# Kernel optimization log

Measured on AMD Instinct MI355X. Metric: run time of the kernel, lower is better.

## Reference

```python
import jax, jax.numpy as jnp
import numpy as np

B, S, D = 2, 2048, 1024
E, K = 8, 2
H = 1792  # round_up(int(1024*5/3)=1706, 256)


def setup_inputs() -> dict:
    key = jax.random.key(0)
    k1, k2, k3, k4, k5 = jax.random.split(key, 5)
    scale = 0.02
    x = jax.random.normal(k1, (B, S, D), dtype=jnp.float32)
    gate_w = jax.random.normal(k2, (E, D), dtype=jnp.float32) * scale   # nn.Linear(D,E).weight
    w_gate = jax.random.normal(k3, (E, D, H), dtype=jnp.float32) * scale
    w_up = jax.random.normal(k4, (E, D, H), dtype=jnp.float32) * scale
    w_down = jax.random.normal(k5, (E, H, D), dtype=jnp.float32) * scale
    return {"x": x, "gate_w": gate_w, "w_gate": w_gate, "w_up": w_up, "w_down": w_down}


def reference(x, gate_w, w_gate, w_up, w_down):
    b, s, d = x.shape
    x_flat = x.reshape(-1, d)                      # [T, D]
    # Gate computed in bf16 (torch autocast) then cast back to f32.
    logits = (x_flat.astype(jnp.bfloat16) @ gate_w.T.astype(jnp.bfloat16)).astype(jnp.float32)  # [T, E]
    topk_w, topk_idx = jax.lax.top_k(logits, K)    # [T, K]
    topk_w = jax.nn.softmax(topk_w, axis=-1)
    probs = jax.nn.softmax(logits, axis=-1)        # [T, E]
    mean_probs = probs.mean(0)                     # [E]
    load_balance_loss = E * jnp.sum(mean_probs ** 2)
    # Per-token combine weight for each expert (equivalent to sort/split/index_add combine).
    combine = jnp.sum(jax.nn.one_hot(topk_idx, E, dtype=x_flat.dtype) * topk_w[..., None], axis=1)  # [T, E]
    out = jnp.zeros_like(x_flat)
    for e in range(E):  # fixed small expert loop; math identical to grouped dispatch
        g = x_flat @ w_gate[e]                     # [T, H]
        u = x_flat @ w_up[e]                       # [T, H]
        y = (jax.nn.silu(g) * u) @ w_down[e]       # [T, D]
        out = out + y * combine[:, e:e + 1]
    return out.reshape(b, s, d), load_balance_loss, mean_probs
```

## Files before the change

kernel.cpp:

```cpp
#include <hip/hip_runtime.h>
#include <stdint.h>

#define TT 4096
#define DD 1024
#define EE 8
#define HH 1792
#define MP 10240
#define MT256 40
#define MT128 80

typedef __attribute__((ext_vector_type(8))) short short8;
typedef __attribute__((ext_vector_type(4))) short short4v;
typedef __attribute__((ext_vector_type(4))) float f32x4;

static __device__ __forceinline__ unsigned short f2bf(float f) {
  union { float f; uint32_t u; } v; v.f = f;
  return (unsigned short)((v.u + 0x7fffu + ((v.u >> 16) & 1u)) >> 16);
}
static __device__ __forceinline__ float bf2f(unsigned short h) {
  union { uint32_t u; float f; } v; v.u = ((uint32_t)h) << 16;
  return v.f;
}

static __device__ __forceinline__ void gll16(const void* g, const void* l) {
  __builtin_amdgcn_global_load_lds(
      (const __attribute__((address_space(1))) unsigned int*)g,
      (__attribute__((address_space(3))) unsigned int*)l, 16, 0, 0);
}

__global__ __launch_bounds__(256) void transpose_convert(
    const float* __restrict__ in, unsigned short* __restrict__ outp, int R, int C,
    int ilv, int sel) {
  __shared__ float t[64][68];
  const float* src = in + (size_t)blockIdx.z * R * C + (size_t)(blockIdx.x * 64) * C +
                     blockIdx.y * 64;
  unsigned short* dst = outp + (size_t)blockIdx.z * R * C * (ilv ? 2 : 1);
  const int tid = threadIdx.x;
  const int lr = tid >> 2, lc = (tid & 3) * 16;
#pragma unroll
  for (int q = 0; q < 4; ++q) {
    const f32x4 v = *(const f32x4*)(src + (size_t)lr * C + lc + 4 * q);
    t[lr][lc + 4 * q + 0] = v[0]; t[lr][lc + 4 * q + 1] = v[1];
    t[lr][lc + 4 * q + 2] = v[2]; t[lr][lc + 4 * q + 3] = v[3];
  }
  __syncthreads();
  unsigned short b[16];
#pragma unroll
  for (int q = 0; q < 16; ++q) b[q] = f2bf(t[lc + q][lr]);
  const int cg = blockIdx.y * 64 + lr;
  const int prow = ilv ? ((cg >> 4) * 32 + sel * 16 + (cg & 15)) : cg;
  unsigned short* d = dst + (size_t)prow * R + blockIdx.x * 64 + lc;
  *(short8*)(d) = *(const short8*)&b[0];
  *(short8*)(d + 8) = *(const short8*)&b[8];
}

__global__ __launch_bounds__(256) void gate_kernel(
    const float* __restrict__ x, const float* __restrict__ gw,
    float* __restrict__ combine, float* __restrict__ probs, int2* __restrict__ topk) {
  const int lane = threadIdx.x & 63;
  const int wave = threadIdx.x >> 6;
  const int t = blockIdx.x * 4 + wave;
  const float* xr = x + (size_t)t * DD;
  float acc[EE];
#pragma unroll
  for (int e = 0; e < EE; ++e) acc[e] = 0.f;
  for (int i = 0; i < DD / 64; ++i) {
    const int d = i * 64 + lane;
    const float xv = bf2f(f2bf(xr[d]));
#pragma unroll
    for (int e = 0; e < EE; ++e)
      acc[e] += xv * bf2f(f2bf(gw[e * DD + d]));
  }
#pragma unroll
  for (int e = 0; e < EE; ++e) {
#pragma unroll
    for (int off = 32; off > 0; off >>= 1)
      acc[e] += __shfl_xor(acc[e], off, 64);
  }
  if (lane == 0) {
    float lg[EE];
#pragma unroll
    for (int e = 0; e < EE; ++e) lg[e] = bf2f(f2bf(acc[e]));
    float m1 = -1e30f, m2 = -1e30f; int i1 = 0, i2 = 0;
#pragma unroll
    for (int e = 0; e < EE; ++e) {
      const float v = lg[e];
      if (v > m1) { m2 = m1; i2 = i1; m1 = v; i1 = e; }
      else if (v > m2) { m2 = v; i2 = e; }
    }
    const float e2 = expf(m2 - m1);
    const float w1 = 1.f / (1.f + e2);
    const float w2 = e2 * w1;
    float cb[EE];
#pragma unroll
    for (int e = 0; e < EE; ++e) cb[e] = 0.f;
    cb[i1] = w1; cb[i2] += w2;
    float p[EE]; float s = 0.f;
#pragma unroll
    for (int e = 0; e < EE; ++e) { p[e] = expf(lg[e] - m1); s += p[e]; }
    const float inv = 1.f / s;
#pragma unroll
    for (int e = 0; e < EE; ++e) {
      combine[(size_t)t * EE + e] = cb[e];
      probs[(size_t)t * EE + e] = p[e] * inv;
    }
    topk[t] = make_int2(i1, i2);
  }
}

__global__ __launch_bounds__(256) void reduce_kernel(
    const float* __restrict__ probs, float* __restrict__ tail) {
  const int tid = threadIdx.x;
  const int lane = tid & 63, wave = tid >> 6;
  float acc[EE];
#pragma unroll
  for (int e = 0; e < EE; ++e) acc[e] = 0.f;
  for (int t = tid; t < TT; t += 256) {
#pragma unroll
    for (int e = 0; e < EE; ++e) acc[e] += probs[(size_t)t * EE + e];
  }
#pragma unroll
  for (int e = 0; e < EE; ++e) {
#pragma unroll
    for (int off = 32; off > 0; off >>= 1)
      acc[e] += __shfl_xor(acc[e], off, 64);
  }
  __shared__ float sm[4][EE];
  if (lane == 0) {
#pragma unroll
    for (int e = 0; e < EE; ++e) sm[wave][e] = acc[e];
  }
  __syncthreads();
  if (tid == 0) {
    float loss = 0.f;
#pragma unroll
    for (int e = 0; e < EE; ++e) {
      const float m = (sm[0][e] + sm[1][e] + sm[2][e] + sm[3][e]) * (1.f / TT);
      tail[1 + e] = m;
      loss += m * m;
    }
    tail[0] = (float)EE * loss;
  }
}

__global__ __launch_bounds__(512) void route_kernel(
    const int2* __restrict__ topk, const float* __restrict__ combine,
    int* __restrict__ tok_list, float* __restrict__ wt_list,
    int* __restrict__ tab256, int* __restrict__ tab128) {
  const int lane = threadIdx.x & 63;
  const int e = threadIdx.x >> 6;
  __shared__ int cnts[EE], offs[EE];
  int cnt = 0;
  for (int i = 0; i < TT / 64; ++i) {
    const int2 k2 = topk[i * 64 + lane];
    cnt += __popcll(__ballot(k2.x == e || k2.y == e));
  }
  if (lane == 0) cnts[e] = cnt;
  __syncthreads();
  if (threadIdx.x == 0) {
    int off = 0, n256 = 0, n128 = 0;
    for (int f = 0; f < EE; ++f) {
      offs[f] = off;
      const int pc = (cnts[f] + 255) & ~255;
      for (int j = 0; j < (pc >> 8); ++j) {
        tab256[2 * n256] = f; tab256[2 * n256 + 1] = off + 256 * j; ++n256;
      }
      for (int j = 0; j < (pc >> 7); ++j) {
        tab128[2 * n128] = f; tab128[2 * n128 + 1] = off + 128 * j; ++n128;
      }
      off += pc;
    }
    for (; n256 < MT256; ++n256) { tab256[2 * n256] = -1; tab256[2 * n256 + 1] = 0; }
    for (; n128 < MT128; ++n128) { tab128[2 * n128] = -1; tab128[2 * n128 + 1] = 0; }
  }
  __syncthreads();
  int pos = offs[e];
  for (int i = 0; i < TT / 64; ++i) {
    const int t = i * 64 + lane;
    const int2 k2 = topk[t];
    const bool sel = (k2.x == e || k2.y == e);
    const unsigned long long m = __ballot(sel);
    if (sel) {
      const int p = pos + __popcll(m & ((1ull << lane) - 1ull));
      tok_list[p] = t;
      wt_list[p] = combine[(size_t)t * EE + e];
    }
    pos += __popcll(m);
  }
  const int pc = (cnt + 255) & ~255;
  for (int s = cnt + lane; s < pc; s += 64) {
    tok_list[offs[e] + s] = 0;
    wt_list[offs[e] + s] = 0.f;
  }
}

__global__ __launch_bounds__(256) void gather_x(
    const float* __restrict__ x, const int* __restrict__ tok_list,
    const int* __restrict__ tab256, unsigned short* __restrict__ xg) {
  const int e = tab256[2 * blockIdx.x];
  if (e < 0) return;
  const int row0 = tab256[2 * blockIdx.x + 1] + blockIdx.y * 16;
  const int tid = threadIdx.x;
#pragma unroll
  for (int i = 0; i < 16; ++i) {
    const int row = row0 + i;
    const int tok = tok_list[row];
    const f32x4 v = *(const f32x4*)(x + (size_t)tok * DD + tid * 4);
    unsigned short b[4] = {f2bf(v[0]), f2bf(v[1]), f2bf(v[2]), f2bf(v[3])};
    *(short4v*)(xg + (size_t)row * DD + tid * 4) = *(const short4v*)b;
  }
}

template <int MODE>
__global__ __launch_bounds__(512, 2) void gemm_main(
    const unsigned short* __restrict__ Ab, const unsigned short* __restrict__ Bb,
    const int* __restrict__ tab, const int* __restrict__ tok_list,
    const float* __restrict__ wt_list, unsigned short* __restrict__ act,
    float* __restrict__ out) {
  constexpr int K      = (MODE == 0) ? DD : HH;
  constexpr int BM     = (MODE == 0) ? 256 : 128;
  constexpr int NBR    = (MODE == 0) ? 2 * HH : DD;
  constexpr int NK     = K / 32;
  constexpr int ABYTES = BM * 64;
  constexpr int SLOTB  = (BM + 256) * 64;
  constexpr int GLL    = SLOTB / 8192;
  constexpr int VCNT   = GLL;
  constexpr int NIT    = ((MODE == 0) ? 128 : 64) / 16;
  constexpr int NNT    = NBR / 256;
  extern __shared__ char lds[];

  const int nwg = gridDim.x;
  const int wgid = (blockIdx.x & 7) * (nwg >> 3) + (blockIdx.x >> 3);
  const int mt = wgid / NNT, nt = wgid % NNT;
  const int e = tab[2 * mt];
  if (e < 0) return;
  const int row0 = tab[2 * mt + 1];
  const int n0 = nt * 256;

  const int tid = threadIdx.x, lane = tid & 63, wave = tid >> 6;
  const int wm = (wave >> 2) * ((MODE == 0) ? 128 : 64);
  const int wn = (wave & 3) * 64;
  const int fr = lane & 15, hi = lane >> 4;

  const unsigned short* At = Ab + (size_t)row0 * K;
  const unsigned short* Bt = Bb + ((size_t)e * NBR + n0) * K;

  asm volatile("s_waitcnt vmcnt(0)" ::: "memory");

  auto stage_q = [&](int u, int slot, int q) {
    const int rel = q * 8192 + wave * 1024 + lane * 16;
    const bool isA = rel < ABYTES;
    const int rb = isA ? rel : rel - ABYTES;
    const int row = rb >> 6;
    const int l = (((rb >> 4) & 3)) ^ ((row >> 1) & 3);
    gll16((isA ? At : Bt) + (size_t)row * K + u * 32 + l * 8,
          lds + slot * SLOTB + q * 8192 + wave * 1024);
  };
  auto rdA = [&](int slot, int m) -> short8 {
    const int c = hi ^ ((m >> 1) & 3);
    return *(const short8*)(lds + slot * SLOTB + m * 64 + (c << 4));
  };
  auto rdB = [&](int slot, int n) -> short8 {
    const int c = hi ^ ((n >> 1) & 3);
    return *(const short8*)(lds + slot * SLOTB + ABYTES + n * 64 + (c << 4));
  };

  f32x4 acc[NIT][4];
#pragma unroll
  for (int i = 0; i < NIT; ++i)
#pragma unroll
    for (int j = 0; j < 4; ++j) acc[i][j] = (f32x4){0.f, 0.f, 0.f, 0.f};

#pragma unroll
  for (int q = 0; q < GLL; ++q) stage_q(0, 0, q);
#pragma unroll
  for (int q = 0; q < GLL; ++q) stage_q(1, 1, q);
  if constexpr (VCNT == 4) asm volatile("s_waitcnt vmcnt(4)" ::: "memory");
  else                     asm volatile("s_waitcnt vmcnt(3)" ::: "memory");
  __builtin_amdgcn_s_barrier();

  int slot = 0;
#pragma unroll 1
  for (int t = 0; t < NK; ++t) {
    const int nslot = (slot >= 1) ? slot - 1 : slot + 2;
    const int u = (t + 2 >= NK) ? t + 2 - NK : t + 2;
    short8 b[4];
    if constexpr (MODE == 0) {
      short8 a[4];
#pragma unroll
      for (int i = 0; i < 4; ++i) a[i] = rdA(slot, wm + i * 16 + fr);
#pragma unroll
      for (int j = 0; j < 4; ++j) b[j] = rdB(slot, wn + j * 16 + fr);
      stage_q(u, nslot, 0); stage_q(u, nslot, 1);
      __builtin_amdgcn_s_barrier();
      asm volatile("s_waitcnt lgkmcnt(0)" ::: "memory");
      __builtin_amdgcn_sched_barrier(0);
      __builtin_amdgcn_s_setprio(1);
#pragma unroll
      for (int i = 0; i < 4; ++i)
#pragma unroll
        for (int j = 0; j < 4; ++j)
          acc[i][j] = __builtin_amdgcn_mfma_f32_16x16x32_bf16(a[i], b[j], acc[i][j], 0, 0, 0);
      __builtin_amdgcn_s_setprio(0);
      __builtin_amdgcn_s_barrier();
#pragma unroll
      for (int i = 0; i < 4; ++i) a[i] = rdA(slot, wm + 64 + i * 16 + fr);
      stage_q(u, nslot, 2); stage_q(u, nslot, 3);
      asm volatile("s_waitcnt vmcnt(4)" ::: "memory");
      __builtin_amdgcn_s_barrier();
      asm volatile("s_waitcnt lgkmcnt(0)" ::: "memory");
      __builtin_amdgcn_sched_barrier(0);
      __builtin_amdgcn_s_setprio(1);
#pragma unroll
      for (int i = 0; i < 4; ++i)
#pragma unroll
        for (int j = 0; j < 4; ++j)
          acc[4 + i][j] = __builtin_amdgcn_mfma_f32_16x16x32_bf16(a[i], b[j], acc[4 + i][j], 0, 0, 0);
      __builtin_amdgcn_s_setprio(0);
      __builtin_amdgcn_s_barrier();
    } else {
      short8 a[4];
#pragma unroll
      for (int i = 0; i < 4; ++i) a[i] = rdA(slot, wm + i * 16 + fr);
#pragma unroll
      for (int j = 0; j < 2; ++j) b[j] = rdB(slot, wn + j * 16 + fr);
      stage_q(u, nslot, 0); stage_q(u, nslot, 1);
      __builtin_amdgcn_s_barrier();
      asm volatile("s_waitcnt lgkmcnt(0)" ::: "memory");
      __builtin_amdgcn_sched_barrier(0);
      __builtin_amdgcn_s_setprio(1);
#pragma unroll
      for (int i = 0; i < 4; ++i)
#pragma unroll
        for (int j = 0; j < 2; ++j)
          acc[i][j] = __builtin_amdgcn_mfma_f32_16x16x32_bf16(a[i], b[j], acc[i][j], 0, 0, 0);
      __builtin_amdgcn_s_setprio(0);
      __builtin_amdgcn_s_barrier();
#pragma unroll
      for (int j = 0; j < 2; ++j) b[2 + j] = rdB(slot, wn + 32 + j * 16 + fr);
      stage_q(u, nslot, 2);
      asm volatile("s_waitcnt vmcnt(3)" ::: "memory");
      __builtin_amdgcn_s_barrier();
      asm volatile("s_waitcnt lgkmcnt(0)" ::: "memory");
      __builtin_amdgcn_sched_barrier(0);
      __builtin_amdgcn_s_setprio(1);
#pragma unroll
      for (int i = 0; i < 4; ++i)
#pragma unroll
        for (int j = 0; j < 2; ++j)
          acc[i][2 + j] = __builtin_amdgcn_mfma_f32_16x16x32_bf16(a[i], b[2 + j], acc[i][2 + j], 0, 0, 0);
      __builtin_amdgcn_s_setprio(0);
      __builtin_amdgcn_s_barrier();
    }
    slot = (slot >= 2) ? 0 : slot + 1;
  }
  asm volatile("s_waitcnt vmcnt(0)" ::: "memory");

  const int r4 = hi * 4;
  if constexpr (MODE == 0) {
#pragma unroll
    for (int i = 0; i < NIT; ++i)
#pragma unroll
      for (int r = 0; r < 4; ++r) {
        const int row = row0 + wm + i * 16 + r4 + r;
#pragma unroll
        for (int jj = 0; jj < 2; ++jj) {
          const float g = acc[i][2 * jj][r], u = acc[i][2 * jj + 1][r];
          const int nb = n0 + wn + jj * 32;
          const int h = ((nb >> 5) << 4) + fr;
          act[(size_t)row * HH + h] = f2bf((g / (1.f + expf(-g))) * u);
        }
      }
  } else {
#pragma unroll
    for (int i = 0; i < NIT; ++i)
#pragma unroll
      for (int r = 0; r < 4; ++r) {
        const int rl = row0 + wm + i * 16 + r4 + r;
        const int tok = tok_list[rl];
        const float wt = wt_list[rl];
        if (wt != 0.f) {
#pragma unroll
          for (int j = 0; j < 4; ++j)
            unsafeAtomicAdd(&out[(size_t)tok * DD + n0 + wn + j * 16 + fr],
                            acc[i][j][r] * wt);
        }
      }
  }
}

extern "C" void kernel_launch(void* const* d_in, const int* in_sizes, int n_in,
                              void* d_out, int out_size, void* d_ws, size_t ws_size,
                              hipStream_t stream) {
  const float* x      = (const float*)d_in[0];
  const float* gw     = (const float*)d_in[1];
  const float* w_gate = (const float*)d_in[2];
  const float* w_up   = (const float*)d_in[3];
  const float* w_down = (const float*)d_in[4];
  float* out = (float*)d_out;
  float* tail = out + (size_t)TT * DD;

  char* w = (char*)d_ws;
  size_t o = 0;
  auto carve = [&](size_t bytes) { char* p = w + o; o += (bytes + 255) & ~255ull; return p; };
  unsigned short* wguT = (unsigned short*)carve((size_t)EE * 2 * HH * DD * 2);
  unsigned short* wdT  = (unsigned short*)carve((size_t)EE * DD * HH * 2);
  unsigned short* xg   = (unsigned short*)carve((size_t)MP * DD * 2);
  unsigned short* act  = (unsigned short*)carve((size_t)MP * HH * 2);
  float* combine = (float*)carve((size_t)TT * EE * 4);
  float* probs   = (float*)carve((size_t)TT * EE * 4);
  int2* topk     = (int2*)carve((size_t)TT * 8);
  int* tok_list  = (int*)carve((size_t)MP * 4);
  float* wt_list = (float*)carve((size_t)MP * 4);
  int* tab256    = (int*)carve((size_t)MT256 * 8);
  int* tab128    = (int*)carve((size_t)MT128 * 8);

  hipMemsetAsync(out, 0, (size_t)TT * DD * sizeof(float), stream);

  transpose_convert<<<dim3(DD / 64, HH / 64, EE), 256, 0, stream>>>(w_gate, wguT, DD, HH, 1, 0);
  transpose_convert<<<dim3(DD / 64, HH / 64, EE), 256, 0, stream>>>(w_up,   wguT, DD, HH, 1, 1);
  transpose_convert<<<dim3(HH / 64, DD / 64, EE), 256, 0, stream>>>(w_down, wdT,  HH, DD, 0, 0);

  gate_kernel<<<TT / 4, 256, 0, stream>>>(x, gw, combine, probs, topk);
  reduce_kernel<<<1, 256, 0, stream>>>(probs, tail);
  route_kernel<<<1, 512, 0, stream>>>(topk, combine, tok_list, wt_list, tab256, tab128);
  gather_x<<<dim3(MT256, 16), 256, 0, stream>>>(x, tok_list, tab256, xg);

  hipFuncSetAttribute(reinterpret_cast<const void*>(&gemm_main<0>),
                      hipFuncAttributeMaxDynamicSharedMemorySize, 98304);
  hipFuncSetAttribute(reinterpret_cast<const void*>(&gemm_main<1>),
                      hipFuncAttributeMaxDynamicSharedMemorySize, 73728);

  gemm_main<0><<<MT256 * 14, 512, 98304, stream>>>(xg, wguT, tab256, nullptr, nullptr, act, nullptr);
  gemm_main<1><<<MT128 * 4, 512, 73728, stream>>>(act, wdT, tab128, tok_list, wt_list, nullptr, out);
}
```

Before: 298.2 us.

## Restructure grouped GEMMs with K=64 double-buffered ping-pong pipeline and 256-row down tiles

```diff
diff --git a/kernel.cpp b/kernel.cpp
--- a/kernel.cpp
+++ b/kernel.cpp
@@ -7,7 +7,6 @@
 #define HH 1792
 #define MP 10240
 #define MT256 40
-#define MT128 80
 
 typedef __attribute__((ext_vector_type(8))) short short8;
 typedef __attribute__((ext_vector_type(4))) short short4v;
@@ -145,8 +144,7 @@
 
 __global__ __launch_bounds__(512) void route_kernel(
     const int2* __restrict__ topk, const float* __restrict__ combine,
-    int* __restrict__ tok_list, float* __restrict__ wt_list,
-    int* __restrict__ tab256, int* __restrict__ tab128) {
+    int* __restrict__ tok_list, float* __restrict__ wt_list, int* __restrict__ tab256) {
   const int lane = threadIdx.x & 63;
   const int e = threadIdx.x >> 6;
   __shared__ int cnts[EE], offs[EE];
@@ -158,20 +156,16 @@
   if (lane == 0) cnts[e] = cnt;
   __syncthreads();
   if (threadIdx.x == 0) {
-    int off = 0, n256 = 0, n128 = 0;
+    int off = 0, n256 = 0;
     for (int f = 0; f < EE; ++f) {
       offs[f] = off;
       const int pc = (cnts[f] + 255) & ~255;
       for (int j = 0; j < (pc >> 8); ++j) {
         tab256[2 * n256] = f; tab256[2 * n256 + 1] = off + 256 * j; ++n256;
       }
-      for (int j = 0; j < (pc >> 7); ++j) {
-        tab128[2 * n128] = f; tab128[2 * n128 + 1] = off + 128 * j; ++n128;
-      }
       off += pc;
     }
     for (; n256 < MT256; ++n256) { tab256[2 * n256] = -1; tab256[2 * n256 + 1] = 0; }
-    for (; n128 < MT128; ++n128) { tab128[2 * n128] = -1; tab128[2 * n128 + 1] = 0; }
   }
   __syncthreads();
   int pos = offs[e];
@@ -211,22 +205,34 @@
   }
 }
 
+#define PH_SYNC(VC)                                         \
+  __builtin_amdgcn_sched_barrier(0);                        \
+  asm volatile("s_waitcnt vmcnt(" #VC ")" ::: "memory");    \
+  __builtin_amdgcn_s_barrier();                             \
+  asm volatile("s_waitcnt lgkmcnt(0)" ::: "memory");        \
+  __builtin_amdgcn_sched_barrier(0);
+#define PH_SYNCN                                            \
+  __builtin_amdgcn_sched_barrier(0);                        \
+  __builtin_amdgcn_s_barrier();                             \
+  asm volatile("s_waitcnt lgkmcnt(0)" ::: "memory");        \
+  __builtin_amdgcn_sched_barrier(0);
+#define PH_END                                              \
+  __builtin_amdgcn_sched_barrier(0);                        \
+  __builtin_amdgcn_s_barrier();
+
 template <int MODE>
-__global__ __launch_bounds__(512, 2) void gemm_main(
+__global__ __launch_bounds__(512, 1) void gemm_main(
     const unsigned short* __restrict__ Ab, const unsigned short* __restrict__ Bb,
     const int* __restrict__ tab, const int* __restrict__ tok_list,
     const float* __restrict__ wt_list, unsigned short* __restrict__ act,
     float* __restrict__ out) {
-  constexpr int K      = (MODE == 0) ? DD : HH;
-  constexpr int BM     = (MODE == 0) ? 256 : 128;
-  constexpr int NBR    = (MODE == 0) ? 2 * HH : DD;
-  constexpr int NK     = K / 32;
-  constexpr int ABYTES = BM * 64;
-  constexpr int SLOTB  = (BM + 256) * 64;
-  constexpr int GLL    = SLOTB / 8192;
-  constexpr int VCNT   = GLL;
-  constexpr int NIT    = ((MODE == 0) ? 128 : 64) / 16;
-  constexpr int NNT    = NBR / 256;
+  constexpr int K    = (MODE == 0) ? DD : HH;
+  constexpr int NK   = K / 64;
+  constexpr int BN   = (MODE == 0) ? 256 : 128;
+  constexpr int NBR  = (MODE == 0) ? 2 * HH : DD;
+  constexpr int NNT  = NBR / BN;
+  constexpr int ABYT = 256 * 128;
+  constexpr int BUFB = ABYT + BN * 128;
   extern __shared__ char lds[];
 
   const int nwg = gridDim.x;
@@ -235,11 +241,11 @@
   const int e = tab[2 * mt];
   if (e < 0) return;
   const int row0 = tab[2 * mt + 1];
-  const int n0 = nt * 256;
+  const int n0 = nt * BN;
 
   const int tid = threadIdx.x, lane = tid & 63, wave = tid >> 6;
-  const int wm = (wave >> 2) * ((MODE == 0) ? 128 : 64);
-  const int wn = (wave & 3) * 64;
+  const int wm = (MODE == 0) ? (wave >> 2) * 128 : (wave >> 1) * 64;
+  const int wn = (MODE == 0) ? (wave & 3) * 64 : (wave & 1) * 64;
   const int fr = lane & 15, hi = lane >> 4;
 
   const unsigned short* At = Ab + (size_t)row0 * K;
@@ -247,112 +253,213 @@
 
   asm volatile("s_waitcnt vmcnt(0)" ::: "memory");
 
-  auto stage_q = [&](int u, int slot, int q) {
-    const int rel = q * 8192 + wave * 1024 + lane * 16;
-    const bool isA = rel < ABYTES;
-    const int rb = isA ? rel : rel - ABYTES;
-    const int row = rb >> 6;
-    const int l = (((rb >> 4) & 3)) ^ ((row >> 1) & 3);
-    gll16((isA ? At : Bt) + (size_t)row * K + u * 32 + l * 8,
-          lds + slot * SLOTB + q * 8192 + wave * 1024);
+  auto stage_half = [&](int u, int p, int h) {
+    const bool isA = (h < 2);
+    const unsigned short* src = isA ? At : Bt;
+    const int rbase = (h & 1) * 128;
+    const int lbase = p * BUFB + (isA ? 0 : ABYT) + rbase * 128;
+#pragma unroll
+    for (int q = 0; q < 2; ++q) {
+      const int rel = q * 8192 + wave * 1024 + lane * 16;
+      const int row = rel >> 7, ch = (rel >> 4) & 7;
+      gll16(src + (size_t)(rbase + row) * K + u * 64 + ((ch ^ (row & 7)) << 3),
+            lds + lbase + q * 8192 + wave * 1024);
+    }
   };
-  auto rdA = [&](int slot, int m) -> short8 {
-    const int c = hi ^ ((m >> 1) & 3);
-    return *(const short8*)(lds + slot * SLOTB + m * 64 + (c << 4));
+  auto rdA = [&](int p, int row, int kc) -> short8 {
+    const int lb = row * 128 + kc * 64 + hi * 16;
+    return *(const short8*)(lds + p * BUFB + (lb ^ ((row & 7) << 4)));
   };
-  auto rdB = [&](int slot, int n) -> short8 {
-    const int c = hi ^ ((n >> 1) & 3);
-    return *(const short8*)(lds + slot * SLOTB + ABYTES + n * 64 + (c << 4));
+  auto rdB = [&](int p, int row, int kc) -> short8 {
+    const int lb = row * 128 + kc * 64 + hi * 16;
+    return *(const short8*)(lds + p * BUFB + ABYT + (lb ^ ((row & 7) << 4)));
   };
 
+  constexpr int NIT = (MODE == 0) ? 8 : 4;
   f32x4 acc[NIT][4];
 #pragma unroll
   for (int i = 0; i < NIT; ++i)
 #pragma unroll
     for (int j = 0; j < 4; ++j) acc[i][j] = (f32x4){0.f, 0.f, 0.f, 0.f};
 
-#pragma unroll
-  for (int q = 0; q < GLL; ++q) stage_q(0, 0, q);
-#pragma unroll
-  for (int q = 0; q < GLL; ++q) stage_q(1, 1, q);
-  if constexpr (VCNT == 4) asm volatile("s_waitcnt vmcnt(4)" ::: "memory");
-  else                     asm volatile("s_waitcnt vmcnt(3)" ::: "memory");
+  if constexpr (MODE == 0) { stage_half(0, 0, 2); stage_half(0, 0, 3); }
+  else                     { stage_half(0, 0, 2); }
+  stage_half(0, 0, 0); stage_half(0, 0, 1);
+  asm volatile("s_waitcnt vmcnt(0)" ::: "memory");
   __builtin_amdgcn_s_barrier();
 
-  int slot = 0;
+  if constexpr (MODE == 0) {
+    short8 rB[2][4][2], rA03[4][2], rA47[2][4][2];
 #pragma unroll 1
-  for (int t = 0; t < NK; ++t) {
-    const int nslot = (slot >= 1) ? slot - 1 : slot + 2;
-    const int u = (t + 2 >= NK) ? t + 2 - NK : t + 2;
-    short8 b[4];
-    if constexpr (MODE == 0) {
-      short8 a[4];
-#pragma unroll
-      for (int i = 0; i < 4; ++i) a[i] = rdA(slot, wm + i * 16 + fr);
-#pragma unroll
-      for (int j = 0; j < 4; ++j) b[j] = rdB(slot, wn + j * 16 + fr);
-      stage_q(u, nslot, 0); stage_q(u, nslot, 1);
-      __builtin_amdgcn_s_barrier();
-      asm volatile("s_waitcnt lgkmcnt(0)" ::: "memory");
-      __builtin_amdgcn_sched_barrier(0);
-      __builtin_amdgcn_s_setprio(1);
-#pragma unroll
-      for (int i = 0; i < 4; ++i)
+    for (int tt = 0; tt < NK; tt += 2) {
+#pragma unroll
+      for (int par = 0; par < 2; ++par) {
+        const int t = tt + par;
+        const int p = par, pn = par ^ 1;
+        const int u = (t + 1 < NK) ? t + 1 : 0;
 #pragma unroll
         for (int j = 0; j < 4; ++j)
-          acc[i][j] = __builtin_amdgcn_mfma_f32_16x16x32_bf16(a[i], b[j], acc[i][j], 0, 0, 0);
-      __builtin_amdgcn_s_setprio(0);
-      __builtin_amdgcn_s_barrier();
-#pragma unroll
-      for (int i = 0; i < 4; ++i) a[i] = rdA(slot, wm + 64 + i * 16 + fr);
-      stage_q(u, nslot, 2); stage_q(u, nslot, 3);
-      asm volatile("s_waitcnt vmcnt(4)" ::: "memory");
-      __builtin_amdgcn_s_barrier();
-      asm volatile("s_waitcnt lgkmcnt(0)" ::: "memory");
-      __builtin_amdgcn_sched_barrier(0);
-      __builtin_amdgcn_s_setprio(1);
-#pragma unroll
-      for (int i = 0; i < 4; ++i)
+#pragma unroll
+          for (int kc = 0; kc < 2; ++kc) rB[p][j][kc] = rdB(p, wn + j * 16 + fr, kc);
+        stage_half(u, pn, 2);
+        PH_SYNC(2)
+        if (t > 0) {
+          __builtin_amdgcn_s_setprio(1);
+#pragma unroll
+          for (int i = 0; i < 4; ++i)
+#pragma unroll
+            for (int j = 0; j < 2; ++j)
+#pragma unroll
+              for (int kc = 0; kc < 2; ++kc)
+                acc[4 + i][j] = __builtin_amdgcn_mfma_f32_16x16x32_bf16(
+                    rA47[pn][i][kc], rB[pn][j][kc], acc[4 + i][j], 0, 0, 0);
+          __builtin_amdgcn_s_setprio(0);
+        }
+        PH_END
+#pragma unroll
+        for (int i = 0; i < 4; ++i)
+#pragma unroll
+          for (int kc = 0; kc < 2; ++kc) rA03[i][kc] = rdA(p, wm + i * 16 + fr, kc);
+        stage_half(u, pn, 3);
+        PH_SYNCN
+        if (t > 0) {
+          __builtin_amdgcn_s_setprio(1);
+#pragma unroll
+          for (int i = 0; i < 4; ++i)
+#pragma unroll
+            for (int j = 0; j < 2; ++j)
+#pragma unroll
+              for (int kc = 0; kc < 2; ++kc)
+                acc[4 + i][2 + j] = __builtin_amdgcn_mfma_f32_16x16x32_bf16(
+                    rA47[pn][i][kc], rB[pn][2 + j][kc], acc[4 + i][2 + j], 0, 0, 0);
+          __builtin_amdgcn_s_setprio(0);
+        }
+        PH_END
+#pragma unroll
+        for (int i = 0; i < 4; ++i)
+#pragma unroll
+          for (int kc = 0; kc < 2; ++kc) rA47[p][i][kc] = rdA(p, wm + 64 + i * 16 + fr, kc);
+        stage_half(u, pn, 0);
+        PH_SYNCN
+        __builtin_amdgcn_s_setprio(1);
+#pragma unroll
+        for (int i = 0; i < 4; ++i)
+#pragma unroll
+          for (int j = 0; j < 2; ++j)
+#pragma unroll
+            for (int kc = 0; kc < 2; ++kc)
+              acc[i][j] = __builtin_amdgcn_mfma_f32_16x16x32_bf16(
+                  rA03[i][kc], rB[p][j][kc], acc[i][j], 0, 0, 0);
+        __builtin_amdgcn_s_setprio(0);
+        PH_END
+        stage_half(u, pn, 1);
+        PH_SYNC(4)
+        __builtin_amdgcn_s_setprio(1);
+#pragma unroll
+        for (int i = 0; i < 4; ++i)
+#pragma unroll
+          for (int j = 0; j < 2; ++j)
+#pragma unroll
+            for (int kc = 0; kc < 2; ++kc)
+              acc[i][2 + j] = __builtin_amdgcn_mfma_f32_16x16x32_bf16(
+                  rA03[i][kc], rB[p][2 + j][kc], acc[i][2 + j], 0, 0, 0);
+        __builtin_amdgcn_s_setprio(0);
+        PH_END
+      }
+    }
+#pragma unroll
+    for (int i = 0; i < 4; ++i)
+#pragma unroll
+      for (int j = 0; j < 4; ++j)
+#pragma unroll
+        for (int kc = 0; kc < 2; ++kc)
+          acc[4 + i][j] = __builtin_amdgcn_mfma_f32_16x16x32_bf16(
+              rA47[1][i][kc], rB[1][j][kc], acc[4 + i][j], 0, 0, 0);
+  } else {
+    short8 rB[2][4][2], rA01[2][2], rA23[2][2][2];
+#pragma unroll 1
+    for (int tt = 0; tt < NK; tt += 2) {
+#pragma unroll
+      for (int par = 0; par < 2; ++par) {
+        const int t = tt + par;
+        const int p = par, pn = par ^ 1;
+        const int u = (t + 1 < NK) ? t + 1 : 0;
 #pragma unroll
         for (int j = 0; j < 4; ++j)
-          acc[4 + i][j] = __builtin_amdgcn_mfma_f32_16x16x32_bf16(a[i], b[j], acc[4 + i][j], 0, 0, 0);
-      __builtin_amdgcn_s_setprio(0);
-      __builtin_amdgcn_s_barrier();
-    } else {
-      short8 a[4];
-#pragma unroll
-      for (int i = 0; i < 4; ++i) a[i] = rdA(slot, wm + i * 16 + fr);
-#pragma unroll
-      for (int j = 0; j < 2; ++j) b[j] = rdB(slot, wn + j * 16 + fr);
-      stage_q(u, nslot, 0); stage_q(u, nslot, 1);
-      __builtin_amdgcn_s_barrier();
-      asm volatile("s_waitcnt lgkmcnt(0)" ::: "memory");
-      __builtin_amdgcn_sched_barrier(0);
-      __builtin_amdgcn_s_setprio(1);
-#pragma unroll
-      for (int i = 0; i < 4; ++i)
-#pragma unroll
-        for (int j = 0; j < 2; ++j)
-          acc[i][j] = __builtin_amdgcn_mfma_f32_16x16x32_bf16(a[i], b[j], acc[i][j], 0, 0, 0);
-      __builtin_amdgcn_s_setprio(0);
-      __builtin_amdgcn_s_barrier();
-#pragma unroll
-      for (int j = 0; j < 2; ++j) b[2 + j] = rdB(slot, wn + 32 + j * 16 + fr);
-      stage_q(u, nslot, 2);
-      asm volatile("s_waitcnt vmcnt(3)" ::: "memory");
-      __builtin_amdgcn_s_barrier();
-      asm volatile("s_waitcnt lgkmcnt(0)" ::: "memory");
-      __builtin_amdgcn_sched_barrier(0);
-      __builtin_amdgcn_s_setprio(1);
-#pragma unroll
-      for (int i = 0; i < 4; ++i)
-#pragma unroll
-        for (int j = 0; j < 2; ++j)
-          acc[i][2 + j] = __builtin_amdgcn_mfma_f32_16x16x32_bf16(a[i], b[2 + j], acc[i][2 + j], 0, 0, 0);
-      __builtin_amdgcn_s_setprio(0);
-      __builtin_amdgcn_s_barrier();
-    }
-    slot = (slot >= 2) ? 0 : slot + 1;
+#pragma unroll
+          for (int kc = 0; kc < 2; ++kc) rB[p][j][kc] = rdB(p, wn + j * 16 + fr, kc);
+        stage_half(u, pn, 2);
+        PH_SYNC(2)
+        if (t > 0) {
+          __builtin_amdgcn_s_setprio(1);
+#pragma unroll
+          for (int i = 0; i < 2; ++i)
+#pragma unroll
+            for (int j = 0; j < 2; ++j)
+#pragma unroll
+              for (int kc = 0; kc < 2; ++kc)
+                acc[2 + i][j] = __builtin_amdgcn_mfma_f32_16x16x32_bf16(
+                    rA23[pn][i][kc], rB[pn][j][kc], acc[2 + i][j], 0, 0, 0);
+          __builtin_amdgcn_s_setprio(0);
+        }
+        PH_END
+#pragma unroll
+        for (int i = 0; i < 2; ++i)
+#pragma unroll
+          for (int kc = 0; kc < 2; ++kc) {
+            rA01[i][kc] = rdA(p, wm + i * 16 + fr, kc);
+            rA23[p][i][kc] = rdA(p, wm + 32 + i * 16 + fr, kc);
+          }
+        stage_half(u, pn, 0);
+        PH_SYNCN
+        if (t > 0) {
+          __builtin_amdgcn_s_setprio(1);
+#pragma unroll
+          for (int i = 0; i < 2; ++i)
+#pragma unroll
+            for (int j = 0; j < 2; ++j)
+#pragma unroll
+              for (int kc = 0; kc < 2; ++kc)
+                acc[2 + i][2 + j] = __builtin_amdgcn_mfma_f32_16x16x32_bf16(
+                    rA23[pn][i][kc], rB[pn][2 + j][kc], acc[2 + i][2 + j], 0, 0, 0);
+          __builtin_amdgcn_s_setprio(0);
+        }
+        PH_END
+        stage_half(u, pn, 1);
+        PH_SYNCN
+        __builtin_amdgcn_s_setprio(1);
+#pragma unroll
+        for (int i = 0; i < 2; ++i)
+#pragma unroll
+          for (int j = 0; j < 2; ++j)
+#pragma unroll
+            for (int kc = 0; kc < 2; ++kc)
+              acc[i][j] = __builtin_amdgcn_mfma_f32_16x16x32_bf16(
+                  rA01[i][kc], rB[p][j][kc], acc[i][j], 0, 0, 0);
+        __builtin_amdgcn_s_setprio(0);
+        PH_END
+        PH_SYNC(4)
+        __builtin_amdgcn_s_setprio(1);
+#pragma unroll
+        for (int i = 0; i < 2; ++i)
+#pragma unroll
+          for (int j = 0; j < 2; ++j)
+#pragma unroll
+            for (int kc = 0; kc < 2; ++kc)
+              acc[i][2 + j] = __builtin_amdgcn_mfma_f32_16x16x32_bf16(
+                  rA01[i][kc], rB[p][2 + j][kc], acc[i][2 + j], 0, 0, 0);
+        __builtin_amdgcn_s_setprio(0);
+        PH_END
+      }
+    }
+#pragma unroll
+    for (int i = 0; i < 2; ++i)
+#pragma unroll
+      for (int j = 0; j < 4; ++j)
+#pragma unroll
+        for (int kc = 0; kc < 2; ++kc)
+          acc[2 + i][j] = __builtin_amdgcn_mfma_f32_16x16x32_bf16(
+              rA23[1][i][kc], rB[1][j][kc], acc[2 + i][j], 0, 0, 0);
   }
   asm volatile("s_waitcnt vmcnt(0)" ::: "memory");
 
@@ -413,7 +520,6 @@
   int* tok_list  = (int*)carve((size_t)MP * 4);
   float* wt_list = (float*)carve((size_t)MP * 4);
   int* tab256    = (int*)carve((size_t)MT256 * 8);
-  int* tab128    = (int*)carve((size_t)MT128 * 8);
 
   hipMemsetAsync(out, 0, (size_t)TT * DD * sizeof(float), stream);
 
@@ -423,14 +529,14 @@
 
   gate_kernel<<<TT / 4, 256, 0, stream>>>(x, gw, combine, probs, topk);
   reduce_kernel<<<1, 256, 0, stream>>>(probs, tail);
-  route_kernel<<<1, 512, 0, stream>>>(topk, combine, tok_list, wt_list, tab256, tab128);
+  route_kernel<<<1, 512, 0, stream>>>(topk, combine, tok_list, wt_list, tab256);
   gather_x<<<dim3(MT256, 16), 256, 0, stream>>>(x, tok_list, tab256, xg);
 
   hipFuncSetAttribute(reinterpret_cast<const void*>(&gemm_main<0>),
+                      hipFuncAttributeMaxDynamicSharedMemorySize, 131072);
+  hipFuncSetAttribute(reinterpret_cast<const void*>(&gemm_main<1>),
                       hipFuncAttributeMaxDynamicSharedMemorySize, 98304);
-  hipFuncSetAttribute(reinterpret_cast<const void*>(&gemm_main<1>),
-                      hipFuncAttributeMaxDynamicSharedMemorySize, 73728);
-
-  gemm_main<0><<<MT256 * 14, 512, 98304, stream>>>(xg, wguT, tab256, nullptr, nullptr, act, nullptr);
-  gemm_main<1><<<MT128 * 4, 512, 73728, stream>>>(act, wdT, tab128, tok_list, wt_list, nullptr, out);
-}
+
+  gemm_main<0><<<MT256 * 14, 512, 131072, stream>>>(xg, wguT, tab256, nullptr, nullptr, act, nullptr);
+  gemm_main<1><<<MT256 * 8, 512, 98304, stream>>>(act, wdT, tab256, tok_list, wt_list, nullptr, out);
+}
```

Measured after the change: 594.1 us. +99.2%, slower.
